# Kernel optimization log

Hardware: AMD Instinct MI355X
Metric: run time of the kernel (lower is better)

Reference implementation:

```python
import jax, jax.numpy as jnp
import numpy as np

B, C, H, W = 8, 512, 48, 48
WSCALE = 0.02  # keep pre-softmax energies in a sane range


def _conv(x, w, b, stride, pad):
    y = jax.lax.conv_general_dilated(
        x, w, (stride, stride), [(pad, pad), (pad, pad)],
        dimension_numbers=("NCHW", "OIHW", "NCHW"))
    return y + b[None, :, None, None]


def setup_inputs() -> dict:
    key = jax.random.key(0)
    ks = jax.random.split(key, 9)
    return {
        "x": jax.random.normal(ks[0], (B, C, H, W), jnp.float32),
        "Wqc": jax.random.normal(ks[1], (2 * C, C, 3, 3), jnp.float32) * WSCALE,
        "bqc": jax.random.normal(ks[2], (2 * C,), jnp.float32) * WSCALE,
        "Wkc": jax.random.normal(ks[3], (C, C, 3, 3), jnp.float32) * WSCALE,
        "bkc": jax.random.normal(ks[4], (C,), jnp.float32) * WSCALE,
        "Wqp": jax.random.normal(ks[5], (C // 8, C, 1, 1), jnp.float32) * WSCALE,
        "bqp": jax.random.normal(ks[6], (C // 8,), jnp.float32) * WSCALE,
        "Wkp": jax.random.normal(ks[7], (C // 8, C, 1, 1), jnp.float32) * WSCALE,
        "bkp": jax.random.normal(ks[8], (C // 8,), jnp.float32) * WSCALE,
    }


def reference(x, Wqc, bqc, Wkc, bkc, Wqp, bqp, Wkp, bkp):
    b, c, h, w = x.shape
    hw = h * w
    # --- channel attention (CAM) on stride-2 downsampled q/k ---
    qc = _conv(x, Wqc, bqc, 2, 1).reshape(b, 2 * c, -1)   # (B, 2C, H'W')
    kc = _conv(x, Wkc, bkc, 2, 1).reshape(b, c, -1)       # (B, C,  H'W')
    energy = jnp.einsum("bqm,bcm->bqc", qc, kc)            # (B, 2C, C)
    # max-subtraction trick from the source: max - energy, then softmax
    energy_new = jnp.max(energy, axis=-1, keepdims=True) - energy
    attn_c = jax.nn.softmax(energy_new, axis=-1)
    xf = x.reshape(b, c, hw)
    out_c = jnp.einsum("bqc,bcn->bqn", attn_c, xf)         # (B, 2C, HW)
    # --- position attention (PAM) ---
    qp = _conv(x, Wqp, bqp, 1, 0).reshape(b, c // 8, hw)   # (B, C/8, HW)
    kp = _conv(x, Wkp, bkp, 1, 0).reshape(b, c // 8, hw)   # (B, C/8, HW)
    energy_p = jnp.einsum("bdn,bdm->bnm", qp, kp)          # (B, HW, HW)
    attn_p = jax.nn.softmax(energy_p, axis=-1)
    # out_c @ attn_p^T
    out_p = jnp.einsum("bqn,bmn->bqm", out_c, attn_p)      # (B, 2C, HW)
    return out_c, out_p.reshape(b, 2 * c, h, w)
```

## Files before the change

### kernel.cpp

```cpp
#include <hip/hip_runtime.h>
#include <hip/hip_bf16.h>

typedef unsigned short u16;
typedef __attribute__((ext_vector_type(8))) _Float16 half8;
typedef __attribute__((ext_vector_type(8))) unsigned short u16x8;
typedef __attribute__((ext_vector_type(4))) float f32x4;

static __device__ __forceinline__ u16 f2h(float v) {
  return __builtin_bit_cast(u16, (_Float16)v);
}
static __device__ __forceinline__ float h2f(u16 u) {
  return (float)__builtin_bit_cast(_Float16, u);
}

static __device__ __forceinline__ void gll16(const void* g, void* l) {
  __builtin_amdgcn_global_load_lds(
      (const __attribute__((address_space(1))) unsigned int*)g,
      (__attribute__((address_space(3))) unsigned int*)l, 16, 0, 0);
}

template <int N>
static __device__ __forceinline__ void wait_vm() {
  if constexpr (N == 0) asm volatile("s_waitcnt vmcnt(0)" ::: "memory");
  else if constexpr (N == 4) asm volatile("s_waitcnt vmcnt(4)" ::: "memory");
  else if constexpr (N == 6) asm volatile("s_waitcnt vmcnt(6)" ::: "memory");
  else asm volatile("s_waitcnt vmcnt(8)" ::: "memory");
}

template <int NBUF, bool ASPLIT, bool BSPLIT, int EPI>
__global__ __launch_bounds__(256) void gemm_bt(
    const u16* __restrict__ A, const u16* __restrict__ Al,
    const u16* __restrict__ B, const u16* __restrict__ Bl,
    float* __restrict__ Cf, u16* __restrict__ Ch, u16* __restrict__ Cl,
    const float* __restrict__ bias0, const float* __restrict__ bias1,
    int biasSplit, int K, int lda, int ldb, int ldc,
    long long sA, long long sB, long long sC) {
  __shared__ __align__(16) u16 smA[NBUF][(ASPLIT ? 2 : 1) * 128 * 32];
  __shared__ __align__(16) u16 smB[NBUF][(BSPLIT ? 2 : 1) * 128 * 32];
  constexpr int G = 4 + (ASPLIT ? 2 : 0) + (BSPLIT ? 2 : 0);
  constexpr int PD = NBUF - 1;

  const int tid = threadIdx.x;
  const int wave = tid >> 6, lane = tid & 63;
  const int wr = wave >> 1, wc = wave & 1;

  const int gx = gridDim.x, gy = gridDim.y;
  int bx, by;
  long long z;
  if (gridDim.z > 1) {
    const int nwg = gx * gy * (int)gridDim.z;
    const int bid = (int)blockIdx.x + gx * ((int)blockIdx.y + gy * (int)blockIdx.z);
    const int w = (bid & 7) * (nwg >> 3) + (bid >> 3);
    bx = w % gx;
    const int rem = w / gx;
    by = rem % gy;
    z = rem / gy;
  } else {
    bx = blockIdx.x;
    by = blockIdx.y;
    z = 0;
  }

  A += z * sA;
  B += z * sB;
  if (ASPLIT) Al += z * sA;
  if (BSPLIT) Bl += z * sB;
  const long long tM = (long long)by * 128;
  const long long tN = (long long)bx * 128;
  const int r4 = lane >> 2, kc = lane & 3;

  const long long arow0 = (tM + wave * 16 + r4) * (long long)lda + kc * 8;
  const long long arow1 = arow0 + 64LL * lda;
  const long long brow0 = (tN + wave * 16 + r4) * (long long)ldb + kc * 8;
  const long long brow1 = brow0 + 64LL * ldb;

  auto stage = [&](int bf, long long ko) {
    u16* dA = &smA[bf][wave * 512];
    u16* dB = &smB[bf][wave * 512];
    gll16(A + arow0 + ko, dA);
    gll16(A + arow1 + ko, dA + 2048);
    gll16(B + brow0 + ko, dB);
    gll16(B + brow1 + ko, dB + 2048);
    if constexpr (ASPLIT) {
      gll16(Al + arow0 + ko, dA + 4096);
      gll16(Al + arow1 + ko, dA + 4096 + 2048);
    }
    if constexpr (BSPLIT) {
      gll16(Bl + brow0 + ko, dB + 4096);
      gll16(Bl + brow1 + ko, dB + 4096 + 2048);
    }
  };

  f32x4 acc[4][4];
#pragma unroll
  for (int i = 0; i < 4; i++)
#pragma unroll
    for (int j = 0; j < 4; j++) acc[i][j] = f32x4{0.f, 0.f, 0.f, 0.f};

  const int quad = lane >> 4, mr = lane & 15;
  const int nk = K >> 5;

  stage(0, 0);
  if constexpr (PD == 2) {
    if (nk > 1) stage(1, 32);
  }

  int cur = 0;
  for (int kt = 0; kt < nk; ++kt) {
    if (PD == 2 && kt < nk - 1) wait_vm<G>(); else wait_vm<0>();
    __builtin_amdgcn_s_barrier();
    asm volatile("" ::: "memory");

    half8 a[4], b[4];
#pragma unroll
    for (int i = 0; i < 4; i++)
      a[i] = *(const half8*)&smA[cur][(wr * 64 + i * 16 + mr) * 32 + quad * 8];
#pragma unroll
    for (int j = 0; j < 4; j++)
      b[j] = *(const half8*)&smB[cur][(wc * 64 + j * 16 + mr) * 32 + quad * 8];

    if (kt + PD < nk) {
      int pf = cur + PD; if (pf >= NBUF) pf -= NBUF;
      stage(pf, (long long)(kt + PD) * 32);
    }

#pragma unroll
    for (int i = 0; i < 4; i++)
#pragma unroll
      for (int j = 0; j < 4; j++)
        acc[i][j] = __builtin_amdgcn_mfma_f32_16x16x32_f16(a[i], b[j], acc[i][j], 0, 0, 0);

    if constexpr (ASPLIT) {
      half8 al[4];
#pragma unroll
      for (int i = 0; i < 4; i++)
        al[i] = *(const half8*)&smA[cur][4096 + (wr * 64 + i * 16 + mr) * 32 + quad * 8];
#pragma unroll
      for (int i = 0; i < 4; i++)
#pragma unroll
        for (int j = 0; j < 4; j++)
          acc[i][j] = __builtin_amdgcn_mfma_f32_16x16x32_f16(al[i], b[j], acc[i][j], 0, 0, 0);
    }
    if constexpr (BSPLIT) {
      half8 bl[4];
#pragma unroll
      for (int j = 0; j < 4; j++)
        bl[j] = *(const half8*)&smB[cur][4096 + (wc * 64 + j * 16 + mr) * 32 + quad * 8];
#pragma unroll
      for (int i = 0; i < 4; i++)
#pragma unroll
        for (int j = 0; j < 4; j++)
          acc[i][j] = __builtin_amdgcn_mfma_f32_16x16x32_f16(a[i], bl[j], acc[i][j], 0, 0, 0);
    }
    cur = (cur == NBUF - 1) ? 0 : cur + 1;
  }

#pragma unroll
  for (int i = 0; i < 4; i++) {
#pragma unroll
    for (int j = 0; j < 4; j++) {
      const long long gn = tN + wc * 64 + j * 16 + mr;
#pragma unroll
      for (int p = 0; p < 4; p++) {
        const long long gm = tM + wr * 64 + i * 16 + quad * 4 + p;
        float v = acc[i][j][p];
        if constexpr (EPI == 1) v += (gm < biasSplit) ? bias0[gm] : bias1[gm - biasSplit];
        if constexpr (EPI == 3) v += (gn < biasSplit) ? bias0[gn] : bias1[gn - biasSplit];
        if constexpr (EPI == 6) v *= bias0[z * biasSplit + gn];
        const long long off = z * sC + gm * ldc + gn;
        if constexpr (EPI == 0 || EPI == 6) {
          Cf[off] = v;
        } else if constexpr (EPI == 1) {
          u16 h = f2h(v);
          Ch[off] = h;
          Cl[off] = f2h(v - h2f(h));
        } else if constexpr (EPI == 2) {
          Cf[off] = v;
          Ch[off] = f2h(v);
        } else if constexpr (EPI == 5) {
          Ch[off] = f2h(__expf(v - 4.0f));
        } else {
          Ch[off] = f2h(v);
        }
      }
    }
  }
  (void)biasSplit;
}

__global__ void im2col_kernel(const u16* __restrict__ xt, u16* __restrict__ Ph) {
  int idx = blockIdx.x * 256 + threadIdx.x;
  int m = idx / 576;
  int r = idx - m * 576;
  int g = r >> 6;
  int c0 = (r & 63) * 8;
  int b = m / 576, t = m - b * 576;
  int oy = t / 24, ox = t - oy * 24;
  int ky = g / 3, kx = g - ky * 3;
  int iy = 2 * oy - 1 + ky, ix = 2 * ox - 1 + kx;
  u16x8 v = u16x8{0, 0, 0, 0, 0, 0, 0, 0};
  if (iy >= 0 && iy < 48 && ix >= 0 && ix < 48)
    v = *(const u16x8*)&xt[((long long)b * 2304 + iy * 48 + ix) * 512 + c0];
  *(u16x8*)&Ph[(long long)m * 4608 + (long long)g * 512 + c0] = v;
}

__global__ void wprep_kernel(const float* __restrict__ Wqc, const float* __restrict__ Wkc,
                             u16* __restrict__ Wh, u16* __restrict__ Wl,
                             const float* __restrict__ Wqp, const float* __restrict__ Wkp,
                             u16* __restrict__ Wp) {
  if (blockIdx.x >= 3456) {
    int idx = (blockIdx.x - 3456) * 256 + threadIdx.x;
    int d = idx >> 9;
    float v = (d < 64) ? Wqp[idx] : Wkp[idx - 64 * 512];
    Wp[idx] = f2h(v);
    return;
  }
  int idx = blockIdx.x * 256 + threadIdx.x;
  int n = idx / 576;
  int r = idx - n * 576;
  int g = r >> 6;
  int c0 = (r & 63) * 8;
  const float* src = (n < 1024)
      ? &Wqc[((long long)n * 512 + c0) * 9 + g]
      : &Wkc[(((long long)n - 1024) * 512 + c0) * 9 + g];
  u16x8 h8, l8;
#pragma unroll
  for (int j = 0; j < 8; j++) {
    float v = src[j * 9];
    u16 h = f2h(v);
    h8[j] = h;
    l8[j] = f2h(v - h2f(h));
  }
  long long out = (long long)n * 4608 + (long long)g * 512 + c0;
  *(u16x8*)&Wh[out] = h8;
  *(u16x8*)&Wl[out] = l8;
}

__global__ void xt_kernel(const float* __restrict__ x, u16* __restrict__ xt,
                          u16* __restrict__ xh) {
  __shared__ float t[32][33];
  int b = blockIdx.z;
  int sp0 = blockIdx.x * 32, c0 = blockIdx.y * 32;
  int tx = threadIdx.x & 31, ty = threadIdx.x >> 5;
#pragma unroll
  for (int k = 0; k < 4; k++) {
    int c = c0 + ty + k * 8;
    long long src = ((long long)(b * 512 + c)) * 2304 + sp0 + tx;
    float v = x[src];
    t[ty + k * 8][tx] = v;
    xh[src] = f2h(v);
  }
  __syncthreads();
#pragma unroll
  for (int k = 0; k < 4; k++) {
    int sp = sp0 + ty + k * 8;
    xt[((long long)b * 2304 + sp) * 512 + c0 + tx] = f2h(t[tx][ty + k * 8]);
  }
}

__global__ void softmax_cam(const float* __restrict__ E, u16* __restrict__ attn) {
  __shared__ float sm[4];
  const long long r = blockIdx.x;
  const float* e = E + r * 512;
  int tid = threadIdx.x, wave = tid >> 6, lane = tid & 63;
  float v0 = e[tid], v1 = e[tid + 256];
  float mn = fminf(v0, v1);
#pragma unroll
  for (int o = 32; o; o >>= 1) mn = fminf(mn, __shfl_xor(mn, o));
  if (lane == 0) sm[wave] = mn;
  __syncthreads();
  mn = fminf(fminf(sm[0], sm[1]), fminf(sm[2], sm[3]));
  float p0 = __expf(mn - v0), p1 = __expf(mn - v1);
  float s = p0 + p1;
#pragma unroll
  for (int o = 32; o; o >>= 1) s += __shfl_xor(s, o);
  __syncthreads();
  if (lane == 0) sm[wave] = s;
  __syncthreads();
  float inv = 1.f / (sm[0] + sm[1] + sm[2] + sm[3]);
  attn[r * 512 + tid] = f2h(p0 * inv);
  attn[r * 512 + tid + 256] = f2h(p1 * inv);
}

__global__ void rowsum_inv(const u16* __restrict__ EP, float* __restrict__ inv) {
  __shared__ float sm[4];
  const long long r = blockIdx.x;
  const u16* e = EP + r * 2304;
  int tid = threadIdx.x, wave = tid >> 6, lane = tid & 63;
  u16x8 m8 = *(const u16x8*)&e[tid * 8];
  float s = 0.f;
#pragma unroll
  for (int k = 0; k < 8; k++) s += h2f(m8[k]);
  if (tid < 32) {
    u16x8 t8 = *(const u16x8*)&e[2048 + tid * 8];
#pragma unroll
    for (int k = 0; k < 8; k++) s += h2f(t8[k]);
  }
#pragma unroll
  for (int o = 32; o; o >>= 1) s += __shfl_xor(s, o);
  if (lane == 0) sm[wave] = s;
  __syncthreads();
  if (tid == 0) inv[r] = 1.f / (sm[0] + sm[1] + sm[2] + sm[3]);
}

extern "C" void kernel_launch(void* const* d_in, const int* in_sizes, int n_in,
                              void* d_out, int out_size, void* d_ws, size_t ws_size,
                              hipStream_t stream) {
  const float* x   = (const float*)d_in[0];
  const float* Wqc = (const float*)d_in[1];
  const float* bqc = (const float*)d_in[2];
  const float* Wkc = (const float*)d_in[3];
  const float* bkc = (const float*)d_in[4];
  const float* Wqp = (const float*)d_in[5];
  const float* bqp = (const float*)d_in[6];
  const float* Wkp = (const float*)d_in[7];
  const float* bkp = (const float*)d_in[8];
  float* outc = (float*)d_out;
  float* outp = outc + 8LL * 1024 * 2304;

  if (ws_size < 195166208ULL) return;

  char* ws = (char*)d_ws;
  u16*   P    = (u16*)(ws + 0);
  u16*   Wh   = (u16*)(ws + 42467328LL);
  u16*   Wl   = (u16*)(ws + 56623104LL);
  u16*   EP   = (u16*)(ws + 0);
  u16*   qcth = (u16*)(ws + 84934656LL);
  u16*   qctl = (u16*)(ws + 99090432LL);
  u16*   pp   = (u16*)(ws + 84934656LL);
  float* E    = (float*)(ws + 113246208LL);
  float* inv  = (float*)(ws + 113246208LL);
  u16*   attn = (u16*)(ws + 130023424LL);
  u16*   xt   = (u16*)(ws + 138412032LL);
  u16*   xh   = (u16*)(ws + 157286400LL);
  u16*   Yt   = (u16*)(ws + 176160768LL);
  u16*   Wp   = (u16*)(ws + 195035136LL);

  xt_kernel<<<dim3(72, 16, 8), 256, 0, stream>>>(x, xt, xh);
  wprep_kernel<<<3712, 256, 0, stream>>>(Wqc, Wkc, Wh, Wl, Wqp, Wkp, Wp);
  im2col_kernel<<<10368, 256, 0, stream>>>(xt, P);

  gemm_bt<2, true, false, 1><<<dim3(36, 12, 1), 256, 0, stream>>>(
      Wh, Wl, P, nullptr, nullptr, qcth, qctl, bqc, bkc, 1024,
      4608, 4608, 4608, 4608, 0, 0, 0);

  gemm_bt<3, true, true, 0><<<dim3(4, 8, 8), 256, 0, stream>>>(
      qcth, qctl, qcth + 1024LL * 4608, qctl + 1024LL * 4608,
      E, nullptr, nullptr,
      nullptr, nullptr, 0, 576, 4608, 4608, 512, 576, 576, 524288);

  softmax_cam<<<8192, 256, 0, stream>>>(E, attn);

  gemm_bt<3, false, false, 0><<<dim3(18, 8, 8), 256, 0, stream>>>(
      attn, nullptr, xt, nullptr, outc, nullptr, nullptr,
      nullptr, nullptr, 0, 512, 512, 512, 2304, 524288, 1179648, 2359296);

  gemm_bt<2, false, false, 3><<<dim3(1, 144, 1), 256, 0, stream>>>(
      xt, nullptr, Wp, nullptr, nullptr, pp, nullptr,
      bqp, bkp, 64, 512, 512, 512, 128, 0, 0, 0);

  gemm_bt<3, false, false, 5><<<dim3(18, 18, 8), 256, 0, stream>>>(
      pp, nullptr, pp + 64, nullptr, nullptr, EP, nullptr,
      nullptr, nullptr, 0, 64, 128, 128, 2304, 294912, 294912, 5308416);

  rowsum_inv<<<18432, 256, 0, stream>>>(EP, inv);

  gemm_bt<3, false, false, 4><<<dim3(4, 18, 8), 256, 0, stream>>>(
      EP, nullptr, xh, nullptr, nullptr, Yt, nullptr,
      nullptr, nullptr, 0, 2304, 2304, 2304, 512, 5308416, 1179648, 1179648);

  gemm_bt<3, false, false, 6><<<dim3(18, 8, 8), 256, 0, stream>>>(
      attn, nullptr, Yt, nullptr, outp, nullptr, nullptr,
      inv, nullptr, 2304, 512, 512, 512, 2304, 524288, 1179648, 2359296);

  (void)in_sizes; (void)n_in; (void)out_size;
}
```

Before: 560.2 us.

## Fuse im2col into conv GEMM loads and row sums into exp epilogue

```diff
diff --git a/kernel.cpp b/kernel.cpp
--- a/kernel.cpp
+++ b/kernel.cpp
@@ -27,7 +27,7 @@
   else asm volatile("s_waitcnt vmcnt(8)" ::: "memory");
 }
 
-template <int NBUF, bool ASPLIT, bool BSPLIT, int EPI>
+template <int NBUF, bool ASPLIT, bool BSPLIT, bool IMCOL, int EPI>
 __global__ __launch_bounds__(256) void gemm_bt(
     const u16* __restrict__ A, const u16* __restrict__ Al,
     const u16* __restrict__ B, const u16* __restrict__ Bl,
@@ -71,16 +71,45 @@
 
   const long long arow0 = (tM + wave * 16 + r4) * (long long)lda + kc * 8;
   const long long arow1 = arow0 + 64LL * lda;
-  const long long brow0 = (tN + wave * 16 + r4) * (long long)ldb + kc * 8;
-  const long long brow1 = brow0 + 64LL * ldb;
+
+  long long brow0 = 0, brow1 = 0;
+  int spb0 = 0, oy20 = 0, ox20 = 0, spb1 = 0, oy21 = 0, ox21 = 0;
+  if constexpr (IMCOL) {
+    const int n0 = (int)tN + wave * 16 + r4;
+    const int b0 = n0 / 576, t0 = n0 - b0 * 576;
+    const int oy0 = t0 / 24, ox0 = t0 - oy0 * 24;
+    spb0 = b0 * 2304; oy20 = 2 * oy0 - 1; ox20 = 2 * ox0 - 1;
+    const int n1 = n0 + 64;
+    const int b1 = n1 / 576, t1 = n1 - b1 * 576;
+    const int oy1 = t1 / 24, ox1 = t1 - oy1 * 24;
+    spb1 = b1 * 2304; oy21 = 2 * oy1 - 1; ox21 = 2 * ox1 - 1;
+  } else {
+    brow0 = (tN + wave * 16 + r4) * (long long)ldb + kc * 8;
+    brow1 = brow0 + 64LL * ldb;
+  }
 
   auto stage = [&](int bf, long long ko) {
     u16* dA = &smA[bf][wave * 512];
     u16* dB = &smB[bf][wave * 512];
     gll16(A + arow0 + ko, dA);
     gll16(A + arow1 + ko, dA + 2048);
-    gll16(B + brow0 + ko, dB);
-    gll16(B + brow1 + ko, dB + 2048);
+    if constexpr (IMCOL) {
+      const int koi = (int)ko;
+      const int g = koi >> 9;
+      const int ky = g / 3, kx = g - ky * 3;
+      const int co = (koi & 511) + kc * 8;
+      const int iy0 = oy20 + ky, ix0 = ox20 + kx;
+      const u16* s0 = ((unsigned)iy0 < 48u && (unsigned)ix0 < 48u)
+          ? B + (((long long)(spb0 + iy0 * 48 + ix0)) << 9) + co : Bl;
+      gll16(s0, dB);
+      const int iy1 = oy21 + ky, ix1 = ox21 + kx;
+      const u16* s1 = ((unsigned)iy1 < 48u && (unsigned)ix1 < 48u)
+          ? B + (((long long)(spb1 + iy1 * 48 + ix1)) << 9) + co : Bl;
+      gll16(s1, dB + 2048);
+    } else {
+      gll16(B + brow0 + ko, dB);
+      gll16(B + brow1 + ko, dB + 2048);
+    }
     if constexpr (ASPLIT) {
       gll16(Al + arow0 + ko, dA + 4096);
       gll16(Al + arow1 + ko, dA + 4096 + 2048);
@@ -155,59 +184,74 @@
     cur = (cur == NBUF - 1) ? 0 : cur + 1;
   }
 
-#pragma unroll
-  for (int i = 0; i < 4; i++) {
-#pragma unroll
-    for (int j = 0; j < 4; j++) {
-      const long long gn = tN + wc * 64 + j * 16 + mr;
-#pragma unroll
-      for (int p = 0; p < 4; p++) {
-        const long long gm = tM + wr * 64 + i * 16 + quad * 4 + p;
-        float v = acc[i][j][p];
-        if constexpr (EPI == 1) v += (gm < biasSplit) ? bias0[gm] : bias1[gm - biasSplit];
-        if constexpr (EPI == 3) v += (gn < biasSplit) ? bias0[gn] : bias1[gn - biasSplit];
-        if constexpr (EPI == 6) v *= bias0[z * biasSplit + gn];
-        const long long off = z * sC + gm * ldc + gn;
-        if constexpr (EPI == 0 || EPI == 6) {
-          Cf[off] = v;
-        } else if constexpr (EPI == 1) {
-          u16 h = f2h(v);
-          Ch[off] = h;
-          Cl[off] = f2h(v - h2f(h));
-        } else if constexpr (EPI == 2) {
-          Cf[off] = v;
-          Ch[off] = f2h(v);
-        } else if constexpr (EPI == 5) {
-          Ch[off] = f2h(__expf(v - 4.0f));
-        } else {
-          Ch[off] = f2h(v);
+  if constexpr (EPI == 5) {
+#pragma unroll
+    for (int i = 0; i < 4; i++) {
+      float rp[4] = {0.f, 0.f, 0.f, 0.f};
+#pragma unroll
+      for (int j = 0; j < 4; j++) {
+        const long long gn = tN + wc * 64 + j * 16 + mr;
+#pragma unroll
+        for (int p = 0; p < 4; p++) {
+          const long long gm = tM + wr * 64 + i * 16 + quad * 4 + p;
+          const float ev = __expf(acc[i][j][p] - 4.0f);
+          Ch[z * sC + gm * ldc + gn] = f2h(ev);
+          rp[p] += ev;
         }
       }
+#pragma unroll
+      for (int p = 0; p < 4; p++)
+#pragma unroll
+        for (int o = 8; o; o >>= 1) rp[p] += __shfl_xor(rp[p], o);
+      if (mr == 0) {
+#pragma unroll
+        for (int p = 0; p < 4; p++) {
+          const long long gm = tM + wr * 64 + i * 16 + quad * 4 + p;
+          Cf[(z * 2304 + gm) * 36 + bx * 2 + wc] = rp[p];
+        }
+      }
+    }
+  } else {
+#pragma unroll
+    for (int i = 0; i < 4; i++) {
+#pragma unroll
+      for (int j = 0; j < 4; j++) {
+        const long long gn = tN + wc * 64 + j * 16 + mr;
+#pragma unroll
+        for (int p = 0; p < 4; p++) {
+          const long long gm = tM + wr * 64 + i * 16 + quad * 4 + p;
+          float v = acc[i][j][p];
+          if constexpr (EPI == 1) v += (gm < biasSplit) ? bias0[gm] : bias1[gm - biasSplit];
+          if constexpr (EPI == 3) v += (gn < biasSplit) ? bias0[gn] : bias1[gn - biasSplit];
+          if constexpr (EPI == 6) v *= bias0[z * biasSplit + gn];
+          const long long off = z * sC + gm * ldc + gn;
+          if constexpr (EPI == 0 || EPI == 6) {
+            Cf[off] = v;
+          } else if constexpr (EPI == 1) {
+            u16 h = f2h(v);
+            Ch[off] = h;
+            Cl[off] = f2h(v - h2f(h));
+          } else if constexpr (EPI == 2) {
+            Cf[off] = v;
+            Ch[off] = f2h(v);
+          } else {
+            Ch[off] = f2h(v);
+          }
+        }
+      }
     }
   }
   (void)biasSplit;
-}
-
-__global__ void im2col_kernel(const u16* __restrict__ xt, u16* __restrict__ Ph) {
-  int idx = blockIdx.x * 256 + threadIdx.x;
-  int m = idx / 576;
-  int r = idx - m * 576;
-  int g = r >> 6;
-  int c0 = (r & 63) * 8;
-  int b = m / 576, t = m - b * 576;
-  int oy = t / 24, ox = t - oy * 24;
-  int ky = g / 3, kx = g - ky * 3;
-  int iy = 2 * oy - 1 + ky, ix = 2 * ox - 1 + kx;
-  u16x8 v = u16x8{0, 0, 0, 0, 0, 0, 0, 0};
-  if (iy >= 0 && iy < 48 && ix >= 0 && ix < 48)
-    v = *(const u16x8*)&xt[((long long)b * 2304 + iy * 48 + ix) * 512 + c0];
-  *(u16x8*)&Ph[(long long)m * 4608 + (long long)g * 512 + c0] = v;
 }
 
 __global__ void wprep_kernel(const float* __restrict__ Wqc, const float* __restrict__ Wkc,
                              u16* __restrict__ Wh, u16* __restrict__ Wl,
                              const float* __restrict__ Wqp, const float* __restrict__ Wkp,
-                             u16* __restrict__ Wp) {
+                             u16* __restrict__ Wp, u16* __restrict__ zp) {
+  if (blockIdx.x == 3712) {
+    if (threadIdx.x < 32) zp[threadIdx.x] = 0;
+    return;
+  }
   if (blockIdx.x >= 3456) {
     int idx = (blockIdx.x - 3456) * 256 + threadIdx.x;
     int d = idx >> 9;
@@ -282,25 +326,13 @@
   attn[r * 512 + tid + 256] = f2h(p1 * inv);
 }
 
-__global__ void rowsum_inv(const u16* __restrict__ EP, float* __restrict__ inv) {
-  __shared__ float sm[4];
-  const long long r = blockIdx.x;
-  const u16* e = EP + r * 2304;
-  int tid = threadIdx.x, wave = tid >> 6, lane = tid & 63;
-  u16x8 m8 = *(const u16x8*)&e[tid * 8];
+__global__ void inv_from_S(const float* __restrict__ Sp, float* __restrict__ inv) {
+  int r = blockIdx.x * 256 + threadIdx.x;
+  const float* p = Sp + (long long)r * 36;
   float s = 0.f;
 #pragma unroll
-  for (int k = 0; k < 8; k++) s += h2f(m8[k]);
-  if (tid < 32) {
-    u16x8 t8 = *(const u16x8*)&e[2048 + tid * 8];
-#pragma unroll
-    for (int k = 0; k < 8; k++) s += h2f(t8[k]);
-  }
-#pragma unroll
-  for (int o = 32; o; o >>= 1) s += __shfl_xor(s, o);
-  if (lane == 0) sm[wave] = s;
-  __syncthreads();
-  if (tid == 0) inv[r] = 1.f / (sm[0] + sm[1] + sm[2] + sm[3]);
+  for (int k = 0; k < 36; k++) s += p[k];
+  inv[r] = 1.f / s;
 }
 
 extern "C" void kernel_launch(void* const* d_in, const int* in_sizes, int n_in,
@@ -321,55 +353,55 @@
   if (ws_size < 195166208ULL) return;
 
   char* ws = (char*)d_ws;
-  u16*   P    = (u16*)(ws + 0);
   u16*   Wh   = (u16*)(ws + 42467328LL);
   u16*   Wl   = (u16*)(ws + 56623104LL);
   u16*   EP   = (u16*)(ws + 0);
   u16*   qcth = (u16*)(ws + 84934656LL);
   u16*   qctl = (u16*)(ws + 99090432LL);
   u16*   pp   = (u16*)(ws + 84934656LL);
+  u16*   zp   = (u16*)(ws + 113246208LL);
   float* E    = (float*)(ws + 113246208LL);
   float* inv  = (float*)(ws + 113246208LL);
   u16*   attn = (u16*)(ws + 130023424LL);
   u16*   xt   = (u16*)(ws + 138412032LL);
+  float* Spart= (float*)(ws + 138412032LL);
   u16*   xh   = (u16*)(ws + 157286400LL);
   u16*   Yt   = (u16*)(ws + 176160768LL);
   u16*   Wp   = (u16*)(ws + 195035136LL);
 
   xt_kernel<<<dim3(72, 16, 8), 256, 0, stream>>>(x, xt, xh);
-  wprep_kernel<<<3712, 256, 0, stream>>>(Wqc, Wkc, Wh, Wl, Wqp, Wkp, Wp);
-  im2col_kernel<<<10368, 256, 0, stream>>>(xt, P);
-
-  gemm_bt<2, true, false, 1><<<dim3(36, 12, 1), 256, 0, stream>>>(
-      Wh, Wl, P, nullptr, nullptr, qcth, qctl, bqc, bkc, 1024,
-      4608, 4608, 4608, 4608, 0, 0, 0);
-
-  gemm_bt<3, true, true, 0><<<dim3(4, 8, 8), 256, 0, stream>>>(
+  wprep_kernel<<<3713, 256, 0, stream>>>(Wqc, Wkc, Wh, Wl, Wqp, Wkp, Wp, zp);
+
+  gemm_bt<2, true, false, true, 1><<<dim3(36, 12, 1), 256, 0, stream>>>(
+      Wh, Wl, xt, zp, nullptr, qcth, qctl, bqc, bkc, 1024,
+      4608, 4608, 512, 4608, 0, 0, 0);
+
+  gemm_bt<3, true, true, false, 0><<<dim3(4, 8, 8), 256, 0, stream>>>(
       qcth, qctl, qcth + 1024LL * 4608, qctl + 1024LL * 4608,
       E, nullptr, nullptr,
       nullptr, nullptr, 0, 576, 4608, 4608, 512, 576, 576, 524288);
 
   softmax_cam<<<8192, 256, 0, stream>>>(E, attn);
 
-  gemm_bt<3, false, false, 0><<<dim3(18, 8, 8), 256, 0, stream>>>(
+  gemm_bt<3, false, false, false, 0><<<dim3(18, 8, 8), 256, 0, stream>>>(
       attn, nullptr, xt, nullptr, outc, nullptr, nullptr,
       nullptr, nullptr, 0, 512, 512, 512, 2304, 524288, 1179648, 2359296);
 
-  gemm_bt<2, false, false, 3><<<dim3(1, 144, 1), 256, 0, stream>>>(
+  gemm_bt<2, false, false, false, 3><<<dim3(1, 144, 1), 256, 0, stream>>>(
       xt, nullptr, Wp, nullptr, nullptr, pp, nullptr,
       bqp, bkp, 64, 512, 512, 512, 128, 0, 0, 0);
 
-  gemm_bt<3, false, false, 5><<<dim3(18, 18, 8), 256, 0, stream>>>(
-      pp, nullptr, pp + 64, nullptr, nullptr, EP, nullptr,
+  gemm_bt<3, false, false, false, 5><<<dim3(18, 18, 8), 256, 0, stream>>>(
+      pp, nullptr, pp + 64, nullptr, Spart, EP, nullptr,
       nullptr, nullptr, 0, 64, 128, 128, 2304, 294912, 294912, 5308416);
 
-  rowsum_inv<<<18432, 256, 0, stream>>>(EP, inv);
-
-  gemm_bt<3, false, false, 4><<<dim3(4, 18, 8), 256, 0, stream>>>(
+  inv_from_S<<<72, 256, 0, stream>>>(Spart, inv);
+
+  gemm_bt<3, false, false, false, 4><<<dim3(4, 18, 8), 256, 0, stream>>>(
       EP, nullptr, xh, nullptr, nullptr, Yt, nullptr,
       nullptr, nullptr, 0, 2304, 2304, 2304, 512, 5308416, 1179648, 1179648);
 
-  gemm_bt<3, false, false, 6><<<dim3(18, 8, 8), 256, 0, stream>>>(
+  gemm_bt<3, false, false, false, 6><<<dim3(18, 8, 8), 256, 0, stream>>>(
       attn, nullptr, Yt, nullptr, outp, nullptr, nullptr,
       inv, nullptr, 2304, 512, 512, 512, 2304, 524288, 1179648, 2359296);
 
```

Result: faster. 549.2 us (-2.0%).
